# Kernel tuning notes

Hardware: AMD Instinct MI355X
Metric: run time of the kernel (lower is better)

## Reference

```python
import jax, jax.numpy as jnp
import numpy as np

N = 50000       # nodes
E = 800000      # directed edges (before self-loops)
IN = 128        # in_channels
H = 8           # heads
C = 32          # hidden_channels (per head)
OUT = 4         # out_channels
NS_ATT = 0.2    # PyG GATConv attention leaky-relu slope
NS_ACT = 0.01   # model activation leaky-relu slope
EPS = 1e-5      # BatchNorm eps


def setup_inputs() -> dict:
    key = jax.random.key(0)
    ks = jax.random.split(key, 18)
    s = 0.05
    return {
        "x": jax.random.normal(ks[0], (N, IN), jnp.float32),
        "edge_index": jax.random.randint(ks[1], (2, E), 0, N, dtype=jnp.int32),
        # layer 1: GATConv(IN -> C, heads=H, concat)
        "W1": jax.random.normal(ks[2], (IN, H * C), jnp.float32) * s,
        "as1": jax.random.normal(ks[3], (H, C), jnp.float32) * s,
        "ad1": jax.random.normal(ks[4], (H, C), jnp.float32) * s,
        "b1": jnp.zeros((H * C,), jnp.float32),
        "g1": jnp.ones((H * C,), jnp.float32),
        "be1": jnp.zeros((H * C,), jnp.float32),
        # middle layer: GATConv(H*C -> C, heads=H, concat) + BN + residual
        "W2": jax.random.normal(ks[5], (H * C, H * C), jnp.float32) * s,
        "as2": jax.random.normal(ks[6], (H, C), jnp.float32) * s,
        "ad2": jax.random.normal(ks[7], (H, C), jnp.float32) * s,
        "b2": jnp.zeros((H * C,), jnp.float32),
        "g2": jnp.ones((H * C,), jnp.float32),
        "be2": jnp.zeros((H * C,), jnp.float32),
        # final layer: GATConv(H*C -> OUT, heads=1, concat=False)
        "W3": jax.random.normal(ks[8], (H * C, OUT), jnp.float32) * s,
        "as3": jax.random.normal(ks[9], (1, OUT), jnp.float32) * s,
        "ad3": jax.random.normal(ks[10], (1, OUT), jnp.float32) * s,
        "b3": jnp.zeros((OUT,), jnp.float32),
    }


def _lrelu(x, slope):
    return jnp.where(x >= 0, x, slope * x)


def _gat_conv(x, src, dst, W, a_src, a_dst, bias, heads, ch, concat):
    # PyG GATConv: h = x @ W per head; edge logit = LReLU(a_src.h_j + a_dst.h_i)
    n = x.shape[0]
    h = (x @ W).reshape(n, heads, ch)                      # [N,H,C]
    al_s = jnp.sum(h * a_src, axis=-1)                     # [N,H]
    al_d = jnp.sum(h * a_dst, axis=-1)                     # [N,H]
    logits = _lrelu(al_s[src] + al_d[dst], NS_ATT)         # [E,H]
    # segment softmax over edges grouped by destination node
    m = jax.ops.segment_max(logits, dst, num_segments=n)   # [N,H]
    e = jnp.exp(logits - m[dst])
    denom = jax.ops.segment_sum(e, dst, num_segments=n)
    alpha = e / (denom[dst] + 1e-16)                       # [E,H]
    out = jax.ops.segment_sum(alpha[:, :, None] * h[src], dst, num_segments=n)  # [N,H,C]
    if concat:
        return out.reshape(n, heads * ch) + bias
    return out.mean(axis=1) + bias


def _bn(x, gamma, beta):
    mu = jnp.mean(x, axis=0)
    var = jnp.mean((x - mu) ** 2, axis=0)
    return (x - mu) * jax.lax.rsqrt(var + EPS) * gamma + beta


def reference(x, edge_index, W1, as1, ad1, b1, g1, be1,
              W2, as2, ad2, b2, g2, be2, W3, as3, ad3, b3):
    n = x.shape[0]
    loops = jnp.arange(n, dtype=edge_index.dtype)          # self-loops (PyG default)
    src = jnp.concatenate([edge_index[0], loops])
    dst = jnp.concatenate([edge_index[1], loops])
    h = _lrelu(_bn(_gat_conv(x, src, dst, W1, as1, ad1, b1, H, C, True), g1, be1), NS_ACT)
    residual = h
    h = _lrelu(_bn(_gat_conv(h, src, dst, W2, as2, ad2, b2, H, C, True), g2, be2), NS_ACT)
    h = h + residual
    return _gat_conv(h, src, dst, W3, as3, ad3, b3, 1, OUT, False)
```

## Files before the change

### kernel.cpp

```cpp
#include <hip/hip_runtime.h>

typedef __attribute__((ext_vector_type(8))) short bf16x8;
typedef __attribute__((ext_vector_type(4))) float f32x4;

__device__ __forceinline__ float lrelu(float x, float s) { return x >= 0.f ? x : s * x; }
__device__ __forceinline__ float b2f(unsigned short u) {
  union { unsigned int i; float f; } v; v.i = ((unsigned int)u) << 16; return v.f;
}
__device__ __forceinline__ float b2f_lo(unsigned int u) {
  union { unsigned int i; float f; } v; v.i = u << 16; return v.f;
}
__device__ __forceinline__ float b2f_hi(unsigned int u) {
  union { unsigned int i; float f; } v; v.i = u & 0xffff0000u; return v.f;
}
__device__ __forceinline__ unsigned short f2b(float f) {
  union { float f; unsigned int i; } v; v.f = f;
  unsigned int r = v.i + 0x7fffu + ((v.i >> 16) & 1u);
  return (unsigned short)(r >> 16);
}
__device__ __forceinline__ unsigned int fbits(float f) {
  union { float f; unsigned int i; } v; v.f = f; return v.i;
}
__device__ __forceinline__ float bitsf(unsigned int u) {
  union { unsigned int i; float f; } v; v.i = u; return v.f;
}

__global__ __launch_bounds__(256) void k_hist(const int* __restrict__ dst, int e,
                                              int* __restrict__ cnt) {
  int i = blockIdx.x * 256 + threadIdx.x;
  if (i < e) atomicAdd(&cnt[dst[i]], 1);
}

__global__ __launch_bounds__(256) void k_bsum(const int* __restrict__ cnt,
                                              int* __restrict__ bsum, int n) {
  const int base = blockIdx.x * 1024;
  const int t = threadIdx.x;
  int s = 0;
#pragma unroll
  for (int i = 0; i < 4; ++i) {
    int idx = base + t + i * 256;
    if (idx < n) s += cnt[idx] + 1;
  }
#pragma unroll
  for (int off = 1; off < 64; off <<= 1) s += __shfl_xor(s, off);
  __shared__ int ws[4];
  const int lane = t & 63, w = t >> 6;
  if (lane == 0) ws[w] = s;
  __syncthreads();
  if (t == 0) bsum[blockIdx.x] = ws[0] + ws[1] + ws[2] + ws[3];
}

__global__ __launch_bounds__(64) void k_scanb(const int* __restrict__ bsum,
                                              int* __restrict__ boff,
                                              int* __restrict__ ptrN, int B) {
  const int lane = threadIdx.x;
  int v = lane < B ? bsum[lane] : 0;
  int incl = v;
#pragma unroll
  for (int off = 1; off < 64; off <<= 1) {
    int u = __shfl_up(incl, off);
    if (lane >= off) incl += u;
  }
  if (lane < B) boff[lane] = incl - v;
  if (lane == 63) *ptrN = incl;
}

__global__ __launch_bounds__(256) void k_scanl(const int* __restrict__ cnt,
                                               const int* __restrict__ boff,
                                               int* __restrict__ ptr,
                                               int* __restrict__ fill, int n) {
  __shared__ int ws[4];
  const int t = threadIdx.x;
  const int base = blockIdx.x * 1024 + t * 4;
  int v0 = base + 0 < n ? cnt[base + 0] + 1 : 0;
  int v1 = base + 1 < n ? cnt[base + 1] + 1 : 0;
  int v2 = base + 2 < n ? cnt[base + 2] + 1 : 0;
  int v3 = base + 3 < n ? cnt[base + 3] + 1 : 0;
  const int tsum = v0 + v1 + v2 + v3;
  const int lane = t & 63, w = t >> 6;
  int incl = tsum;
#pragma unroll
  for (int off = 1; off < 64; off <<= 1) {
    int u = __shfl_up(incl, off);
    if (lane >= off) incl += u;
  }
  if (lane == 63) ws[w] = incl;
  __syncthreads();
  int excl = boff[blockIdx.x] + incl - tsum;
  for (int i = 0; i < w; ++i) excl += ws[i];
  if (base + 0 < n) { ptr[base + 0] = excl; fill[base + 0] = excl; }
  excl += v0;
  if (base + 1 < n) { ptr[base + 1] = excl; fill[base + 1] = excl; }
  excl += v1;
  if (base + 2 < n) { ptr[base + 2] = excl; fill[base + 2] = excl; }
  excl += v2;
  if (base + 3 < n) { ptr[base + 3] = excl; fill[base + 3] = excl; }
}

__global__ __launch_bounds__(256) void k_scatter(const int* __restrict__ srce,
                                                 const int* __restrict__ dste,
                                                 int e, int n,
                                                 int* __restrict__ fill,
                                                 int* __restrict__ srcs) {
  int i = blockIdx.x * 256 + threadIdx.x;
  if (i < e) {
    int pos = atomicAdd(&fill[dste[i]], 1);
    srcs[pos] = srce[i];
  } else if (i < e + n) {
    int v = i - e;
    int pos = atomicAdd(&fill[v], 1);
    srcs[pos] = v;
  }
}

__global__ __launch_bounds__(256) void k_prep(const float* __restrict__ x,
                                              unsigned short* __restrict__ xb,
                                              const float* __restrict__ W1,
                                              unsigned short* __restrict__ w1t,
                                              const float* __restrict__ W2,
                                              unsigned short* __restrict__ w2t, int n4) {
  int i = blockIdx.x * 256 + threadIdx.x;
  if (i < n4) {
    float4 v = ((const float4*)x)[i];
    ushort4 o;
    o.x = f2b(v.x); o.y = f2b(v.y); o.z = f2b(v.z); o.w = f2b(v.w);
    ((ushort4*)xb)[i] = o;
    return;
  }
  i -= n4;
  if (i < 256 * 128) {
    int nn = i / 128, k = i - nn * 128;
    w1t[i] = f2b(W1[(size_t)k * 256 + nn]);
    return;
  }
  i -= 256 * 128;
  if (i < 256 * 256) {
    int nn = i / 256, k = i - nn * 256;
    w2t[i] = f2b(W2[(size_t)k * 256 + nn]);
  }
}

__global__ __launch_bounds__(256) void k_mfma(const unsigned short* __restrict__ A,
                                              const unsigned short* __restrict__ BT,
                                              unsigned short* __restrict__ C,
                                              const float* __restrict__ as_,
                                              const float* __restrict__ ad_,
                                              float* __restrict__ als,
                                              float* __restrict__ ald,
                                              int M, int Nn, int K) {
  __shared__ unsigned int Asu[128 * 20];
  __shared__ unsigned int Bsu[128 * 20];
  const int tid = threadIdx.x;
  const int bm = blockIdx.x * 128, bn = blockIdx.y * 128;
  const int w = tid >> 6, lane = tid & 63;
  const int wm = w >> 1, wn = w & 1;
  const int l16 = lane & 15, lg = lane >> 4;
  f32x4 acc[4][4] = {};
  for (int k0 = 0; k0 < K; k0 += 32) {
#pragma unroll
    for (int rep = 0; rep < 2; ++rep) {
      int ci = tid + rep * 256;
      int row = ci >> 2, cg = ci & 3;
      int ar = bm + row;
      ar = ar < M ? ar : M - 1;
      uint4 av = *(const uint4*)(A + (size_t)ar * K + k0 + cg * 8);
      *(uint4*)&Asu[row * 20 + cg * 4] = av;
      uint4 bv = *(const uint4*)(BT + (size_t)(bn + row) * K + k0 + cg * 8);
      *(uint4*)&Bsu[row * 20 + cg * 4] = bv;
    }
    __syncthreads();
    bf16x8 aF[4], bF[4];
#pragma unroll
    for (int mi = 0; mi < 4; ++mi)
      aF[mi] = *(const bf16x8*)&Asu[(wm * 64 + mi * 16 + l16) * 20 + lg * 4];
#pragma unroll
    for (int ni = 0; ni < 4; ++ni)
      bF[ni] = *(const bf16x8*)&Bsu[(wn * 64 + ni * 16 + l16) * 20 + lg * 4];
#pragma unroll
    for (int mi = 0; mi < 4; ++mi)
#pragma unroll
      for (int ni = 0; ni < 4; ++ni)
        acc[mi][ni] =
            __builtin_amdgcn_mfma_f32_16x16x32_bf16(aF[mi], bF[ni], acc[mi][ni], 0, 0, 0);
    __syncthreads();
  }
  float asv[4], adv[4];
#pragma unroll
  for (int ni = 0; ni < 4; ++ni) {
    int gcol = bn + wn * 64 + ni * 16 + l16;
    asv[ni] = as_[gcol];
    adv[ni] = ad_[gcol];
  }
  const int hb = (bn >> 5) + wn * 2;
#pragma unroll
  for (int mi = 0; mi < 4; ++mi) {
#pragma unroll
    for (int r = 0; r < 4; ++r) {
      int grow = bm + wm * 64 + mi * 16 + lg * 4 + r;
      bool ok = grow < M;
      if (ok) {
#pragma unroll
        for (int ni = 0; ni < 4; ++ni) {
          int gcol = bn + wn * 64 + ni * 16 + l16;
          C[(size_t)grow * Nn + gcol] = f2b(acc[mi][ni][r]);
        }
      }
      float ps0 = acc[mi][0][r] * asv[0] + acc[mi][1][r] * asv[1];
      float ps1 = acc[mi][2][r] * asv[2] + acc[mi][3][r] * asv[3];
      float pd0 = acc[mi][0][r] * adv[0] + acc[mi][1][r] * adv[1];
      float pd1 = acc[mi][2][r] * adv[2] + acc[mi][3][r] * adv[3];
#pragma unroll
      for (int off = 1; off < 16; off <<= 1) {
        ps0 += __shfl_xor(ps0, off);
        ps1 += __shfl_xor(ps1, off);
        pd0 += __shfl_xor(pd0, off);
        pd1 += __shfl_xor(pd1, off);
      }
      if (ok && l16 == 0) {
        *(float2*)(als + (size_t)grow * 8 + hb) = make_float2(ps0, ps1);
        *(float2*)(ald + (size_t)grow * 8 + hb) = make_float2(pd0, pd1);
      }
    }
  }
}

__global__ __launch_bounds__(256) void k_agg(const unsigned short* __restrict__ h,
                                             const float* __restrict__ als,
                                             const float* __restrict__ ald,
                                             const int* __restrict__ ptr,
                                             const int* __restrict__ srcs,
                                             const float* __restrict__ bias,
                                             unsigned short* __restrict__ out, int n) {
  int wid = (blockIdx.x * 256 + threadIdx.x) >> 6;
  int lane = threadIdx.x & 63;
  if (wid >= n) return;
  const int beg = ptr[wid], end = ptr[wid + 1];
  const int L = lane & 15;
  const int e = lane >> 4;
  const int hh = L >> 1;
  const float adh = ald[(size_t)wid * 8 + hh];
  float s = 0.f;
  float a0 = 0, a1 = 0, a2 = 0, a3 = 0, a4 = 0, a5 = 0, a6 = 0, a7 = 0;
  float a8 = 0, a9 = 0, aA = 0, aB = 0, aC = 0, aD = 0, aE = 0, aF = 0;
  int j = beg + e;
  int s0 = j < end ? srcs[j] : 0;
  int s1 = (j + 4) < end ? srcs[j + 4] : 0;
  const uint4* hp0 = (const uint4*)(h + (size_t)s0 * 256 + L * 16);
  uint4 c0 = hp0[0];
  uint4 c1 = hp0[1];
  float alsc = als[(size_t)s0 * 8 + hh];
  for (; j < end; j += 4) {
    int s2 = (j + 8) < end ? srcs[j + 8] : 0;
    const uint4* hp1 = (const uint4*)(h + (size_t)s1 * 256 + L * 16);
    uint4 n0 = hp1[0];
    uint4 n1 = hp1[1];
    float alsn = als[(size_t)s1 * 8 + hh];
    float lg = lrelu(alsc + adh, 0.2f);
    float wt = __expf(lg);
    s += wt;
    a0 += wt * b2f_lo(c0.x); a1 += wt * b2f_hi(c0.x);
    a2 += wt * b2f_lo(c0.y); a3 += wt * b2f_hi(c0.y);
    a4 += wt * b2f_lo(c0.z); a5 += wt * b2f_hi(c0.z);
    a6 += wt * b2f_lo(c0.w); a7 += wt * b2f_hi(c0.w);
    a8 += wt * b2f_lo(c1.x); a9 += wt * b2f_hi(c1.x);
    aA += wt * b2f_lo(c1.y); aB += wt * b2f_hi(c1.y);
    aC += wt * b2f_lo(c1.z); aD += wt * b2f_hi(c1.z);
    aE += wt * b2f_lo(c1.w); aF += wt * b2f_hi(c1.w);
    c0 = n0; c1 = n1; alsc = alsn;
    s1 = s2;
  }
  a0 += __shfl_xor(a0, 16); a0 += __shfl_xor(a0, 32);
  a1 += __shfl_xor(a1, 16); a1 += __shfl_xor(a1, 32);
  a2 += __shfl_xor(a2, 16); a2 += __shfl_xor(a2, 32);
  a3 += __shfl_xor(a3, 16); a3 += __shfl_xor(a3, 32);
  a4 += __shfl_xor(a4, 16); a4 += __shfl_xor(a4, 32);
  a5 += __shfl_xor(a5, 16); a5 += __shfl_xor(a5, 32);
  a6 += __shfl_xor(a6, 16); a6 += __shfl_xor(a6, 32);
  a7 += __shfl_xor(a7, 16); a7 += __shfl_xor(a7, 32);
  a8 += __shfl_xor(a8, 16); a8 += __shfl_xor(a8, 32);
  a9 += __shfl_xor(a9, 16); a9 += __shfl_xor(a9, 32);
  aA += __shfl_xor(aA, 16); aA += __shfl_xor(aA, 32);
  aB += __shfl_xor(aB, 16); aB += __shfl_xor(aB, 32);
  aC += __shfl_xor(aC, 16); aC += __shfl_xor(aC, 32);
  aD += __shfl_xor(aD, 16); aD += __shfl_xor(aD, 32);
  aE += __shfl_xor(aE, 16); aE += __shfl_xor(aE, 32);
  aF += __shfl_xor(aF, 16); aF += __shfl_xor(aF, 32);
  s += __shfl_xor(s, 16); s += __shfl_xor(s, 32);
  const float inv = 1.f / (s + 1e-16f);
  if (e == 0) {
    const float4* bp = (const float4*)(bias + L * 16);
    float4 b0 = bp[0], b1 = bp[1], b2 = bp[2], b3 = bp[3];
    uint4 o0, o1;
    o0.x = (unsigned int)f2b(a0 * inv + b0.x) | ((unsigned int)f2b(a1 * inv + b0.y) << 16);
    o0.y = (unsigned int)f2b(a2 * inv + b0.z) | ((unsigned int)f2b(a3 * inv + b0.w) << 16);
    o0.z = (unsigned int)f2b(a4 * inv + b1.x) | ((unsigned int)f2b(a5 * inv + b1.y) << 16);
    o0.w = (unsigned int)f2b(a6 * inv + b1.z) | ((unsigned int)f2b(a7 * inv + b1.w) << 16);
    o1.x = (unsigned int)f2b(a8 * inv + b2.x) | ((unsigned int)f2b(a9 * inv + b2.y) << 16);
    o1.y = (unsigned int)f2b(aA * inv + b2.z) | ((unsigned int)f2b(aB * inv + b2.w) << 16);
    o1.z = (unsigned int)f2b(aC * inv + b3.x) | ((unsigned int)f2b(aD * inv + b3.y) << 16);
    o1.w = (unsigned int)f2b(aE * inv + b3.z) | ((unsigned int)f2b(aF * inv + b3.w) << 16);
    uint4* op = (uint4*)(out + (size_t)wid * 256 + L * 16);
    op[0] = o0;
    op[1] = o1;
  }
}

__global__ __launch_bounds__(256) void k_bnp1(const unsigned short* __restrict__ x,
                                              float* __restrict__ partial, int n) {
  const int t = threadIdx.x;
  const int q = t & 63;
  const int rsub = t >> 6;
  float s0 = 0, s1 = 0, s2 = 0, s3 = 0, q0 = 0, q1 = 0, q2 = 0, q3 = 0;
  int r = blockIdx.x * 4 + rsub;
  for (; r + 6144 < n; r += 8192) {
    ushort4 va = *(const ushort4*)(x + (size_t)r * 256 + q * 4);
    ushort4 vb = *(const ushort4*)(x + (size_t)(r + 2048) * 256 + q * 4);
    ushort4 vc = *(const ushort4*)(x + (size_t)(r + 4096) * 256 + q * 4);
    ushort4 vd = *(const ushort4*)(x + (size_t)(r + 6144) * 256 + q * 4);
    float f;
    f = b2f(va.x); s0 += f; q0 += f * f;
    f = b2f(va.y); s1 += f; q1 += f * f;
    f = b2f(va.z); s2 += f; q2 += f * f;
    f = b2f(va.w); s3 += f; q3 += f * f;
    f = b2f(vb.x); s0 += f; q0 += f * f;
    f = b2f(vb.y); s1 += f; q1 += f * f;
    f = b2f(vb.z); s2 += f; q2 += f * f;
    f = b2f(vb.w); s3 += f; q3 += f * f;
    f = b2f(vc.x); s0 += f; q0 += f * f;
    f = b2f(vc.y); s1 += f; q1 += f * f;
    f = b2f(vc.z); s2 += f; q2 += f * f;
    f = b2f(vc.w); s3 += f; q3 += f * f;
    f = b2f(vd.x); s0 += f; q0 += f * f;
    f = b2f(vd.y); s1 += f; q1 += f * f;
    f = b2f(vd.z); s2 += f; q2 += f * f;
    f = b2f(vd.w); s3 += f; q3 += f * f;
  }
  for (; r < n; r += 2048) {
    ushort4 v = *(const ushort4*)(x + (size_t)r * 256 + q * 4);
    float f;
    f = b2f(v.x); s0 += f; q0 += f * f;
    f = b2f(v.y); s1 += f; q1 += f * f;
    f = b2f(v.z); s2 += f; q2 += f * f;
    f = b2f(v.w); s3 += f; q3 += f * f;
  }
  __shared__ float ls[4][512];
  ls[rsub][q * 4 + 0] = s0; ls[rsub][q * 4 + 1] = s1;
  ls[rsub][q * 4 + 2] = s2; ls[rsub][q * 4 + 3] = s3;
  ls[rsub][256 + q * 4 + 0] = q0; ls[rsub][256 + q * 4 + 1] = q1;
  ls[rsub][256 + q * 4 + 2] = q2; ls[rsub][256 + q * 4 + 3] = q3;
  __syncthreads();
  float a = ls[0][t] + ls[1][t] + ls[2][t] + ls[3][t];
  float b = ls[0][256 + t] + ls[1][256 + t] + ls[2][256 + t] + ls[3][256 + t];
  partial[blockIdx.x * 512 + t] = a;
  partial[blockIdx.x * 512 + 256 + t] = b;
}

__global__ __launch_bounds__(256) void k_bnp2(const float* __restrict__ partial,
                                              const float* __restrict__ ga,
                                              const float* __restrict__ be,
                                              float* __restrict__ ss, float invn) {
  const int c = blockIdx.x * 4 + (threadIdx.x >> 6);
  const int lane = threadIdx.x & 63;
  float s = 0.f, qq = 0.f;
#pragma unroll
  for (int k = 0; k < 8; ++k) {
    int b = lane + k * 64;
    s += partial[(size_t)b * 512 + c];
    qq += partial[(size_t)b * 512 + 256 + c];
  }
#pragma unroll
  for (int off = 1; off < 64; off <<= 1) {
    s += __shfl_xor(s, off);
    qq += __shfl_xor(qq, off);
  }
  if (lane == 0) {
    float mu = s * invn;
    float var = qq * invn - mu * mu;
    float sc = ga[c] * rsqrtf(var + 1e-5f);
    ss[c] = sc;
    ss[256 + c] = be[c] - mu * sc;
  }
}

__global__ __launch_bounds__(256) void k_bnact(const unsigned short* __restrict__ x,
                                               const float* __restrict__ ss,
                                               unsigned short* __restrict__ out, int n) {
  const int tot4 = n * 64;
  for (int t = blockIdx.x * 256 + threadIdx.x; t < tot4; t += gridDim.x * 256) {
    int i0 = t * 4;
    int c = i0 & 255;
    ushort4 xu = *(const ushort4*)(x + i0);
    float4 scv = *(const float4*)(ss + c);
    float4 shv = *(const float4*)(ss + 256 + c);
    float t0 = b2f(xu.x) * scv.x + shv.x;
    float t1 = b2f(xu.y) * scv.y + shv.y;
    float t2 = b2f(xu.z) * scv.z + shv.z;
    float t3 = b2f(xu.w) * scv.w + shv.w;
    float o0 = fmaxf(t0, 0.01f * t0);
    float o1 = fmaxf(t1, 0.01f * t1);
    float o2 = fmaxf(t2, 0.01f * t2);
    float o3 = fmaxf(t3, 0.01f * t3);
    ushort4 ob;
    ob.x = f2b(o0); ob.y = f2b(o1); ob.z = f2b(o2); ob.w = f2b(o3);
    *(ushort4*)(out + i0) = ob;
  }
}

__global__ __launch_bounds__(256) void k_bnact3(const unsigned short* __restrict__ x,
                                                const float* __restrict__ ss,
                                                const unsigned short* __restrict__ res,
                                                const float* __restrict__ W3,
                                                const float* __restrict__ as3,
                                                const float* __restrict__ ad3,
                                                uint4* __restrict__ h3p, int n) {
  int wid = (blockIdx.x * 256 + threadIdx.x) >> 6;
  int lane = threadIdx.x & 63;
  if (wid >= n) return;
  const int c = lane * 4;
  ushort4 xu = *(const ushort4*)(x + (size_t)wid * 256 + c);
  ushort4 rv = *(const ushort4*)(res + (size_t)wid * 256 + c);
  float4 scv = *(const float4*)(ss + c);
  float4 shv = *(const float4*)(ss + 256 + c);
  float t0 = b2f(xu.x) * scv.x + shv.x;
  float t1 = b2f(xu.y) * scv.y + shv.y;
  float t2 = b2f(xu.z) * scv.z + shv.z;
  float t3 = b2f(xu.w) * scv.w + shv.w;
  float o0 = fmaxf(t0, 0.01f * t0) + b2f(rv.x);
  float o1 = fmaxf(t1, 0.01f * t1) + b2f(rv.y);
  float o2 = fmaxf(t2, 0.01f * t2) + b2f(rv.z);
  float o3 = fmaxf(t3, 0.01f * t3) + b2f(rv.w);
  const float4* Wp = (const float4*)W3 + lane * 4;
  float4 w0 = Wp[0], w1 = Wp[1], w2 = Wp[2], w3 = Wp[3];
  float a0 = o0 * w0.x + o1 * w1.x + o2 * w2.x + o3 * w3.x;
  float a1 = o0 * w0.y + o1 * w1.y + o2 * w2.y + o3 * w3.y;
  float a2 = o0 * w0.z + o1 * w1.z + o2 * w2.z + o3 * w3.z;
  float a3 = o0 * w0.w + o1 * w1.w + o2 * w2.w + o3 * w3.w;
#pragma unroll
  for (int off = 1; off < 64; off <<= 1) {
    a0 += __shfl_xor(a0, off);
    a1 += __shfl_xor(a1, off);
    a2 += __shfl_xor(a2, off);
    a3 += __shfl_xor(a3, off);
  }
  if (lane == 0) {
    float als3v = a0 * as3[0] + a1 * as3[1] + a2 * as3[2] + a3 * as3[3];
    float ald3v = a0 * ad3[0] + a1 * ad3[1] + a2 * ad3[2] + a3 * ad3[3];
    uint4 pv;
    pv.x = (unsigned int)f2b(a0) | ((unsigned int)f2b(a1) << 16);
    pv.y = (unsigned int)f2b(a2) | ((unsigned int)f2b(a3) << 16);
    pv.z = fbits(als3v);
    pv.w = fbits(ald3v);
    h3p[wid] = pv;
  }
}

__global__ __launch_bounds__(256) void k_agg3(const uint4* __restrict__ h3p,
                                              const int* __restrict__ ptr,
                                              const int* __restrict__ srcs,
                                              const float* __restrict__ b3,
                                              float* __restrict__ out, int n) {
  int wid = (blockIdx.x * 256 + threadIdx.x) >> 6;
  int lane = threadIdx.x & 63;
  if (wid >= n) return;
  const int beg = ptr[wid], end = ptr[wid + 1];
  const float aldh = bitsf(h3p[wid].w);
  float s = 0.f, a0 = 0.f, a1 = 0.f, a2 = 0.f, a3 = 0.f;
  for (int j = beg + lane; j < end; j += 64) {
    uint4 v = h3p[srcs[j]];
    float wgt = __expf(lrelu(bitsf(v.z) + aldh, 0.2f));
    s += wgt;
    a0 += wgt * b2f_lo(v.x);
    a1 += wgt * b2f_hi(v.x);
    a2 += wgt * b2f_lo(v.y);
    a3 += wgt * b2f_hi(v.y);
  }
#pragma unroll
  for (int off = 1; off < 64; off <<= 1) {
    s += __shfl_xor(s, off);
    a0 += __shfl_xor(a0, off);
    a1 += __shfl_xor(a1, off);
    a2 += __shfl_xor(a2, off);
    a3 += __shfl_xor(a3, off);
  }
  if (lane == 0) {
    float inv = 1.f / (s + 1e-16f);
    out[(size_t)wid * 4 + 0] = a0 * inv + b3[0];
    out[(size_t)wid * 4 + 1] = a1 * inv + b3[1];
    out[(size_t)wid * 4 + 2] = a2 * inv + b3[2];
    out[(size_t)wid * 4 + 3] = a3 * inv + b3[3];
  }
}

extern "C" void kernel_launch(void* const* d_in, const int* in_sizes, int n_in,
                              void* d_out, int out_size, void* d_ws, size_t ws_size,
                              hipStream_t stream) {
  const float* x   = (const float*)d_in[0];
  const int*   ei  = (const int*)d_in[1];
  const float* W1  = (const float*)d_in[2];
  const float* as1 = (const float*)d_in[3];
  const float* ad1 = (const float*)d_in[4];
  const float* b1  = (const float*)d_in[5];
  const float* ga1 = (const float*)d_in[6];
  const float* be1 = (const float*)d_in[7];
  const float* W2  = (const float*)d_in[8];
  const float* as2 = (const float*)d_in[9];
  const float* ad2 = (const float*)d_in[10];
  const float* b2  = (const float*)d_in[11];
  const float* ga2 = (const float*)d_in[12];
  const float* be2 = (const float*)d_in[13];
  const float* W3  = (const float*)d_in[14];
  const float* as3 = (const float*)d_in[15];
  const float* ad3 = (const float*)d_in[16];
  const float* b3  = (const float*)d_in[17];

  const int N = in_sizes[0] / 128;
  const int E = in_sizes[1] / 2;
  const int ET = E + N;
  float* out = (float*)d_out;

  char* w = (char*)d_ws;
  auto alloc = [&](size_t bytes) -> void* {
    void* p = (void*)w;
    w += (bytes + 255) & ~(size_t)255;
    return p;
  };
  int* ptr              = (int*)alloc((size_t)(N + 1) * 4);
  int* fill             = (int*)alloc((size_t)N * 4);
  int* cnt              = (int*)alloc((size_t)N * 4);
  int* bsum             = (int*)alloc(64 * 4);
  int* boff             = (int*)alloc(64 * 4);
  int* srcs             = (int*)alloc((size_t)ET * 4);
  unsigned short* hbuf  = (unsigned short*)alloc((size_t)N * 256 * 2);
  unsigned short* aggb  = (unsigned short*)alloc((size_t)N * 256 * 2);
  unsigned short* a1b   = (unsigned short*)alloc((size_t)N * 256 * 2);
  unsigned short* xb    = (unsigned short*)alloc((size_t)N * 128 * 2);
  unsigned short* w1t   = (unsigned short*)alloc(256 * 128 * 2);
  unsigned short* w2t   = (unsigned short*)alloc(256 * 256 * 2);
  float* als            = (float*)alloc((size_t)N * 8 * 4);
  float* ald            = (float*)alloc((size_t)N * 8 * 4);
  uint4* h3p            = (uint4*)alloc((size_t)N * 16);
  float* partial        = (float*)alloc(512 * 512 * 4);
  float* ss             = (float*)alloc(1024 * 4);

  const int* esrc = ei;
  const int* edst = ei + E;
  const float invn = 1.f / (float)N;

  hipMemsetAsync(cnt, 0, (size_t)N * 4, stream);

  const int B = (N + 1023) / 1024;
  k_hist<<<(E + 255) / 256, 256, 0, stream>>>(edst, E, cnt);
  k_bsum<<<B, 256, 0, stream>>>(cnt, bsum, N);
  k_scanb<<<1, 64, 0, stream>>>(bsum, boff, ptr + N, B);
  k_scanl<<<B, 256, 0, stream>>>(cnt, boff, ptr, fill, N);
  k_scatter<<<(ET + 255) / 256, 256, 0, stream>>>(esrc, edst, E, N, fill, srcs);

  const int n4 = N * 32;
  const int prep_tot = n4 + 256 * 128 + 256 * 256;
  k_prep<<<(prep_tot + 255) / 256, 256, 0, stream>>>(x, xb, W1, w1t, W2, w2t, n4);

  const dim3 gemm_grid((N + 127) / 128, 2);
  const int wblocks = (N + 3) / 4;

  k_mfma<<<gemm_grid, 256, 0, stream>>>(xb, w1t, hbuf, as1, ad1, als, ald, N, 256, 128);
  k_agg<<<wblocks, 256, 0, stream>>>(hbuf, als, ald, ptr, srcs, b1, aggb, N);
  k_bnp1<<<512, 256, 0, stream>>>(aggb, partial, N);
  k_bnp2<<<64, 256, 0, stream>>>(partial, ga1, be1, ss, invn);
  k_bnact<<<2048, 256, 0, stream>>>(aggb, ss, a1b, N);

  k_mfma<<<gemm_grid, 256, 0, stream>>>(a1b, w2t, hbuf, as2, ad2, als, ald, N, 256, 256);
  k_agg<<<wblocks, 256, 0, stream>>>(hbuf, als, ald, ptr, srcs, b2, aggb, N);
  k_bnp1<<<512, 256, 0, stream>>>(aggb, partial, N);
  k_bnp2<<<64, 256, 0, stream>>>(partial, ga2, be2, ss + 512, invn);
  k_bnact3<<<wblocks, 256, 0, stream>>>(aggb, ss + 512, a1b, W3, as3, ad3, h3p, N);

  k_agg3<<<wblocks, 256, 0, stream>>>(h3p, ptr, srcs, b3, out, N);
}
```

Before: 376.5 us.

## Fuse CSR build and BatchNorm stages into persistent kernels with grid barriers

Replaces the histogram, scan, scatter and bf16 prep kernels with one persistent 512-block kernel that uses software grid-wide barriers between phases. The two BatchNorm partial, finalize and apply kernel triples are also each fused into one persistent kernel with grid barriers. The aim is to remove many small kernel launches and their gaps. The cost is atomic spin barriers, whose correctness depends on all 512 blocks being co-resident, and the CSR phases now run on fewer threads than before.

```diff
diff --git a/kernel.cpp b/kernel.cpp
--- a/kernel.cpp
+++ b/kernel.cpp
@@ -25,118 +25,134 @@
   union { unsigned int i; float f; } v; v.i = u; return v.f;
 }
 
-__global__ __launch_bounds__(256) void k_hist(const int* __restrict__ dst, int e,
-                                              int* __restrict__ cnt) {
-  int i = blockIdx.x * 256 + threadIdx.x;
-  if (i < e) atomicAdd(&cnt[dst[i]], 1);
-}
-
-__global__ __launch_bounds__(256) void k_bsum(const int* __restrict__ cnt,
-                                              int* __restrict__ bsum, int n) {
-  const int base = blockIdx.x * 1024;
-  const int t = threadIdx.x;
-  int s = 0;
-#pragma unroll
-  for (int i = 0; i < 4; ++i) {
-    int idx = base + t + i * 256;
-    if (idx < n) s += cnt[idx] + 1;
-  }
-#pragma unroll
-  for (int off = 1; off < 64; off <<= 1) s += __shfl_xor(s, off);
+__device__ __forceinline__ void gbar(int* bar, int nb) {
+  __syncthreads();
+  if (threadIdx.x == 0) {
+    __threadfence();
+    int s0 = __hip_atomic_load(&bar[1], __ATOMIC_RELAXED, __HIP_MEMORY_SCOPE_AGENT);
+    int old = __hip_atomic_fetch_add(&bar[0], 1, __ATOMIC_ACQ_REL, __HIP_MEMORY_SCOPE_AGENT);
+    if (old == nb - 1) {
+      __hip_atomic_store(&bar[0], 0, __ATOMIC_RELAXED, __HIP_MEMORY_SCOPE_AGENT);
+      __hip_atomic_fetch_add(&bar[1], 1, __ATOMIC_RELEASE, __HIP_MEMORY_SCOPE_AGENT);
+    } else {
+      while (__hip_atomic_load(&bar[1], __ATOMIC_ACQUIRE, __HIP_MEMORY_SCOPE_AGENT) == s0) {}
+    }
+    __threadfence();
+  }
+  __syncthreads();
+}
+
+__global__ __launch_bounds__(256, 2) void k_csr(int* __restrict__ bar,
+                                                int* __restrict__ cnt,
+                                                const int* __restrict__ esrc,
+                                                const int* __restrict__ edst,
+                                                int E, int N,
+                                                const float* __restrict__ x,
+                                                unsigned short* __restrict__ xb,
+                                                const float* __restrict__ W1,
+                                                unsigned short* __restrict__ w1t,
+                                                const float* __restrict__ W2,
+                                                unsigned short* __restrict__ w2t,
+                                                int* __restrict__ bsum,
+                                                int* __restrict__ ptr,
+                                                int* __restrict__ fill,
+                                                int* __restrict__ srcs) {
+  const int NB = gridDim.x;
+  const int g0 = blockIdx.x * 256 + threadIdx.x;
+  const int gs = NB * 256;
+  const int n4 = N * 32;
   __shared__ int ws[4];
-  const int lane = t & 63, w = t >> 6;
-  if (lane == 0) ws[w] = s;
-  __syncthreads();
-  if (t == 0) bsum[blockIdx.x] = ws[0] + ws[1] + ws[2] + ws[3];
-}
-
-__global__ __launch_bounds__(64) void k_scanb(const int* __restrict__ bsum,
-                                              int* __restrict__ boff,
-                                              int* __restrict__ ptrN, int B) {
-  const int lane = threadIdx.x;
-  int v = lane < B ? bsum[lane] : 0;
-  int incl = v;
-#pragma unroll
-  for (int off = 1; off < 64; off <<= 1) {
-    int u = __shfl_up(incl, off);
-    if (lane >= off) incl += u;
-  }
-  if (lane < B) boff[lane] = incl - v;
-  if (lane == 63) *ptrN = incl;
-}
-
-__global__ __launch_bounds__(256) void k_scanl(const int* __restrict__ cnt,
-                                               const int* __restrict__ boff,
-                                               int* __restrict__ ptr,
-                                               int* __restrict__ fill, int n) {
-  __shared__ int ws[4];
-  const int t = threadIdx.x;
-  const int base = blockIdx.x * 1024 + t * 4;
-  int v0 = base + 0 < n ? cnt[base + 0] + 1 : 0;
-  int v1 = base + 1 < n ? cnt[base + 1] + 1 : 0;
-  int v2 = base + 2 < n ? cnt[base + 2] + 1 : 0;
-  int v3 = base + 3 < n ? cnt[base + 3] + 1 : 0;
-  const int tsum = v0 + v1 + v2 + v3;
-  const int lane = t & 63, w = t >> 6;
-  int incl = tsum;
-#pragma unroll
-  for (int off = 1; off < 64; off <<= 1) {
-    int u = __shfl_up(incl, off);
-    if (lane >= off) incl += u;
-  }
-  if (lane == 63) ws[w] = incl;
-  __syncthreads();
-  int excl = boff[blockIdx.x] + incl - tsum;
-  for (int i = 0; i < w; ++i) excl += ws[i];
-  if (base + 0 < n) { ptr[base + 0] = excl; fill[base + 0] = excl; }
-  excl += v0;
-  if (base + 1 < n) { ptr[base + 1] = excl; fill[base + 1] = excl; }
-  excl += v1;
-  if (base + 2 < n) { ptr[base + 2] = excl; fill[base + 2] = excl; }
-  excl += v2;
-  if (base + 3 < n) { ptr[base + 3] = excl; fill[base + 3] = excl; }
-}
-
-__global__ __launch_bounds__(256) void k_scatter(const int* __restrict__ srce,
-                                                 const int* __restrict__ dste,
-                                                 int e, int n,
-                                                 int* __restrict__ fill,
-                                                 int* __restrict__ srcs) {
-  int i = blockIdx.x * 256 + threadIdx.x;
-  if (i < e) {
-    int pos = atomicAdd(&fill[dste[i]], 1);
-    srcs[pos] = srce[i];
-  } else if (i < e + n) {
-    int v = i - e;
-    int pos = atomicAdd(&fill[v], 1);
-    srcs[pos] = v;
-  }
-}
-
-__global__ __launch_bounds__(256) void k_prep(const float* __restrict__ x,
-                                              unsigned short* __restrict__ xb,
-                                              const float* __restrict__ W1,
-                                              unsigned short* __restrict__ w1t,
-                                              const float* __restrict__ W2,
-                                              unsigned short* __restrict__ w2t, int n4) {
-  int i = blockIdx.x * 256 + threadIdx.x;
-  if (i < n4) {
+  __shared__ int bo_s;
+
+  for (int i = g0; i < N; i += gs) cnt[i] = 0;
+  for (int i = g0; i < n4; i += gs) {
     float4 v = ((const float4*)x)[i];
     ushort4 o;
     o.x = f2b(v.x); o.y = f2b(v.y); o.z = f2b(v.z); o.w = f2b(v.w);
     ((ushort4*)xb)[i] = o;
-    return;
-  }
-  i -= n4;
-  if (i < 256 * 128) {
-    int nn = i / 128, k = i - nn * 128;
+  }
+  for (int i = g0; i < 256 * 128; i += gs) {
+    int nn = i >> 7, k = i & 127;
     w1t[i] = f2b(W1[(size_t)k * 256 + nn]);
-    return;
-  }
-  i -= 256 * 128;
-  if (i < 256 * 256) {
-    int nn = i / 256, k = i - nn * 256;
+  }
+  for (int i = g0; i < 256 * 256; i += gs) {
+    int nn = i >> 8, k = i & 255;
     w2t[i] = f2b(W2[(size_t)k * 256 + nn]);
+  }
+  gbar(bar, NB);
+
+  for (int i = g0; i < E; i += gs) atomicAdd(&cnt[edst[i]], 1);
+  gbar(bar, NB);
+
+  const int B = (N + 1023) >> 10;
+  const int t = threadIdx.x;
+  if (blockIdx.x < B) {
+    const int base = blockIdx.x * 1024;
+    int s = 0;
+#pragma unroll
+    for (int i2 = 0; i2 < 4; ++i2) {
+      int idx = base + t + i2 * 256;
+      if (idx < N) s += cnt[idx] + 1;
+    }
+#pragma unroll
+    for (int off = 1; off < 64; off <<= 1) s += __shfl_xor(s, off);
+    const int lane = t & 63, w = t >> 6;
+    if (lane == 0) ws[w] = s;
+    __syncthreads();
+    if (t == 0) bsum[blockIdx.x] = ws[0] + ws[1] + ws[2] + ws[3];
+  }
+  gbar(bar, NB);
+
+  if (blockIdx.x < B) {
+    if (t < 64) {
+      int v = t < B ? bsum[t] : 0;
+      int incl = v;
+#pragma unroll
+      for (int off = 1; off < 64; off <<= 1) {
+        int u = __shfl_up(incl, off);
+        if (t >= off) incl += u;
+      }
+      if (t == blockIdx.x) bo_s = incl - v;
+      if (blockIdx.x == 0 && t == 63) ptr[N] = incl;
+    }
+    const int base = blockIdx.x * 1024 + t * 4;
+    int v0 = base + 0 < N ? cnt[base + 0] + 1 : 0;
+    int v1 = base + 1 < N ? cnt[base + 1] + 1 : 0;
+    int v2 = base + 2 < N ? cnt[base + 2] + 1 : 0;
+    int v3 = base + 3 < N ? cnt[base + 3] + 1 : 0;
+    const int tsum = v0 + v1 + v2 + v3;
+    const int lane = t & 63, w = t >> 6;
+    int incl = tsum;
+#pragma unroll
+    for (int off = 1; off < 64; off <<= 1) {
+      int u = __shfl_up(incl, off);
+      if (lane >= off) incl += u;
+    }
+    if (lane == 63) ws[w] = incl;
+    __syncthreads();
+    int excl = bo_s + incl - tsum;
+    for (int i = 0; i < w; ++i) excl += ws[i];
+    if (base + 0 < N) { ptr[base + 0] = excl; fill[base + 0] = excl; }
+    excl += v0;
+    if (base + 1 < N) { ptr[base + 1] = excl; fill[base + 1] = excl; }
+    excl += v1;
+    if (base + 2 < N) { ptr[base + 2] = excl; fill[base + 2] = excl; }
+    excl += v2;
+    if (base + 3 < N) { ptr[base + 3] = excl; fill[base + 3] = excl; }
+  }
+  gbar(bar, NB);
+
+  for (int i = g0; i < E + N; i += gs) {
+    if (i < E) {
+      int d = edst[i];
+      int sv = esrc[i];
+      int pos = atomicAdd(&fill[d], 1);
+      __builtin_nontemporal_store(sv, &srcs[pos]);
+    } else {
+      int v = i - E;
+      int pos = atomicAdd(&fill[v], 1);
+      __builtin_nontemporal_store(v, &srcs[pos]);
+    }
   }
 }
 
@@ -305,152 +321,235 @@
   }
 }
 
-__global__ __launch_bounds__(256) void k_bnp1(const unsigned short* __restrict__ x,
-                                              float* __restrict__ partial, int n) {
+__global__ __launch_bounds__(256, 2) void k_bn1(int* __restrict__ bar,
+                                                const unsigned short* __restrict__ xa,
+                                                float* __restrict__ partial,
+                                                const float* __restrict__ ga,
+                                                const float* __restrict__ be,
+                                                float* __restrict__ ss, float invn,
+                                                unsigned short* __restrict__ outb, int n) {
+  const int NB = gridDim.x;
   const int t = threadIdx.x;
-  const int q = t & 63;
-  const int rsub = t >> 6;
-  float s0 = 0, s1 = 0, s2 = 0, s3 = 0, q0 = 0, q1 = 0, q2 = 0, q3 = 0;
-  int r = blockIdx.x * 4 + rsub;
-  for (; r + 6144 < n; r += 8192) {
-    ushort4 va = *(const ushort4*)(x + (size_t)r * 256 + q * 4);
-    ushort4 vb = *(const ushort4*)(x + (size_t)(r + 2048) * 256 + q * 4);
-    ushort4 vc = *(const ushort4*)(x + (size_t)(r + 4096) * 256 + q * 4);
-    ushort4 vd = *(const ushort4*)(x + (size_t)(r + 6144) * 256 + q * 4);
-    float f;
-    f = b2f(va.x); s0 += f; q0 += f * f;
-    f = b2f(va.y); s1 += f; q1 += f * f;
-    f = b2f(va.z); s2 += f; q2 += f * f;
-    f = b2f(va.w); s3 += f; q3 += f * f;
-    f = b2f(vb.x); s0 += f; q0 += f * f;
-    f = b2f(vb.y); s1 += f; q1 += f * f;
-    f = b2f(vb.z); s2 += f; q2 += f * f;
-    f = b2f(vb.w); s3 += f; q3 += f * f;
-    f = b2f(vc.x); s0 += f; q0 += f * f;
-    f = b2f(vc.y); s1 += f; q1 += f * f;
-    f = b2f(vc.z); s2 += f; q2 += f * f;
-    f = b2f(vc.w); s3 += f; q3 += f * f;
-    f = b2f(vd.x); s0 += f; q0 += f * f;
-    f = b2f(vd.y); s1 += f; q1 += f * f;
-    f = b2f(vd.z); s2 += f; q2 += f * f;
-    f = b2f(vd.w); s3 += f; q3 += f * f;
-  }
-  for (; r < n; r += 2048) {
-    ushort4 v = *(const ushort4*)(x + (size_t)r * 256 + q * 4);
-    float f;
-    f = b2f(v.x); s0 += f; q0 += f * f;
-    f = b2f(v.y); s1 += f; q1 += f * f;
-    f = b2f(v.z); s2 += f; q2 += f * f;
-    f = b2f(v.w); s3 += f; q3 += f * f;
-  }
-  __shared__ float ls[4][512];
-  ls[rsub][q * 4 + 0] = s0; ls[rsub][q * 4 + 1] = s1;
-  ls[rsub][q * 4 + 2] = s2; ls[rsub][q * 4 + 3] = s3;
-  ls[rsub][256 + q * 4 + 0] = q0; ls[rsub][256 + q * 4 + 1] = q1;
-  ls[rsub][256 + q * 4 + 2] = q2; ls[rsub][256 + q * 4 + 3] = q3;
-  __syncthreads();
-  float a = ls[0][t] + ls[1][t] + ls[2][t] + ls[3][t];
-  float b = ls[0][256 + t] + ls[1][256 + t] + ls[2][256 + t] + ls[3][256 + t];
-  partial[blockIdx.x * 512 + t] = a;
-  partial[blockIdx.x * 512 + 256 + t] = b;
-}
-
-__global__ __launch_bounds__(256) void k_bnp2(const float* __restrict__ partial,
-                                              const float* __restrict__ ga,
-                                              const float* __restrict__ be,
-                                              float* __restrict__ ss, float invn) {
-  const int c = blockIdx.x * 4 + (threadIdx.x >> 6);
-  const int lane = threadIdx.x & 63;
-  float s = 0.f, qq = 0.f;
-#pragma unroll
-  for (int k = 0; k < 8; ++k) {
-    int b = lane + k * 64;
-    s += partial[(size_t)b * 512 + c];
-    qq += partial[(size_t)b * 512 + 256 + c];
-  }
-#pragma unroll
-  for (int off = 1; off < 64; off <<= 1) {
-    s += __shfl_xor(s, off);
-    qq += __shfl_xor(qq, off);
-  }
-  if (lane == 0) {
-    float mu = s * invn;
-    float var = qq * invn - mu * mu;
-    float sc = ga[c] * rsqrtf(var + 1e-5f);
-    ss[c] = sc;
-    ss[256 + c] = be[c] - mu * sc;
-  }
-}
-
-__global__ __launch_bounds__(256) void k_bnact(const unsigned short* __restrict__ x,
-                                               const float* __restrict__ ss,
-                                               unsigned short* __restrict__ out, int n) {
-  const int tot4 = n * 64;
-  for (int t = blockIdx.x * 256 + threadIdx.x; t < tot4; t += gridDim.x * 256) {
-    int i0 = t * 4;
-    int c = i0 & 255;
-    ushort4 xu = *(const ushort4*)(x + i0);
-    float4 scv = *(const float4*)(ss + c);
-    float4 shv = *(const float4*)(ss + 256 + c);
-    float t0 = b2f(xu.x) * scv.x + shv.x;
-    float t1 = b2f(xu.y) * scv.y + shv.y;
-    float t2 = b2f(xu.z) * scv.z + shv.z;
-    float t3 = b2f(xu.w) * scv.w + shv.w;
-    float o0 = fmaxf(t0, 0.01f * t0);
-    float o1 = fmaxf(t1, 0.01f * t1);
-    float o2 = fmaxf(t2, 0.01f * t2);
-    float o3 = fmaxf(t3, 0.01f * t3);
-    ushort4 ob;
-    ob.x = f2b(o0); ob.y = f2b(o1); ob.z = f2b(o2); ob.w = f2b(o3);
-    *(ushort4*)(out + i0) = ob;
-  }
-}
-
-__global__ __launch_bounds__(256) void k_bnact3(const unsigned short* __restrict__ x,
-                                                const float* __restrict__ ss,
+  {
+    const int q = t & 63;
+    const int rsub = t >> 6;
+    float s0 = 0, s1 = 0, s2 = 0, s3 = 0, q0 = 0, q1 = 0, q2 = 0, q3 = 0;
+    int r = blockIdx.x * 4 + rsub;
+    for (; r + 6144 < n; r += 8192) {
+      ushort4 va = *(const ushort4*)(xa + (size_t)r * 256 + q * 4);
+      ushort4 vb = *(const ushort4*)(xa + (size_t)(r + 2048) * 256 + q * 4);
+      ushort4 vc = *(const ushort4*)(xa + (size_t)(r + 4096) * 256 + q * 4);
+      ushort4 vd = *(const ushort4*)(xa + (size_t)(r + 6144) * 256 + q * 4);
+      float f;
+      f = b2f(va.x); s0 += f; q0 += f * f;
+      f = b2f(va.y); s1 += f; q1 += f * f;
+      f = b2f(va.z); s2 += f; q2 += f * f;
+      f = b2f(va.w); s3 += f; q3 += f * f;
+      f = b2f(vb.x); s0 += f; q0 += f * f;
+      f = b2f(vb.y); s1 += f; q1 += f * f;
+      f = b2f(vb.z); s2 += f; q2 += f * f;
+      f = b2f(vb.w); s3 += f; q3 += f * f;
+      f = b2f(vc.x); s0 += f; q0 += f * f;
+      f = b2f(vc.y); s1 += f; q1 += f * f;
+      f = b2f(vc.z); s2 += f; q2 += f * f;
+      f = b2f(vc.w); s3 += f; q3 += f * f;
+      f = b2f(vd.x); s0 += f; q0 += f * f;
+      f = b2f(vd.y); s1 += f; q1 += f * f;
+      f = b2f(vd.z); s2 += f; q2 += f * f;
+      f = b2f(vd.w); s3 += f; q3 += f * f;
+    }
+    for (; r < n; r += 2048) {
+      ushort4 v = *(const ushort4*)(xa + (size_t)r * 256 + q * 4);
+      float f;
+      f = b2f(v.x); s0 += f; q0 += f * f;
+      f = b2f(v.y); s1 += f; q1 += f * f;
+      f = b2f(v.z); s2 += f; q2 += f * f;
+      f = b2f(v.w); s3 += f; q3 += f * f;
+    }
+    __shared__ float ls[4][512];
+    ls[rsub][q * 4 + 0] = s0; ls[rsub][q * 4 + 1] = s1;
+    ls[rsub][q * 4 + 2] = s2; ls[rsub][q * 4 + 3] = s3;
+    ls[rsub][256 + q * 4 + 0] = q0; ls[rsub][256 + q * 4 + 1] = q1;
+    ls[rsub][256 + q * 4 + 2] = q2; ls[rsub][256 + q * 4 + 3] = q3;
+    __syncthreads();
+    float a = ls[0][t] + ls[1][t] + ls[2][t] + ls[3][t];
+    float b = ls[0][256 + t] + ls[1][256 + t] + ls[2][256 + t] + ls[3][256 + t];
+    partial[blockIdx.x * 512 + t] = a;
+    partial[blockIdx.x * 512 + 256 + t] = b;
+  }
+  gbar(bar, NB);
+  if (blockIdx.x < 64) {
+    const int c = blockIdx.x * 4 + (t >> 6);
+    const int lane = t & 63;
+    float s = 0.f, qq = 0.f;
+#pragma unroll
+    for (int k = 0; k < 8; ++k) {
+      int b = lane + k * 64;
+      s += partial[(size_t)b * 512 + c];
+      qq += partial[(size_t)b * 512 + 256 + c];
+    }
+#pragma unroll
+    for (int off = 1; off < 64; off <<= 1) {
+      s += __shfl_xor(s, off);
+      qq += __shfl_xor(qq, off);
+    }
+    if (lane == 0) {
+      float mu = s * invn;
+      float var = qq * invn - mu * mu;
+      float sc = ga[c] * rsqrtf(var + 1e-5f);
+      ss[c] = sc;
+      ss[256 + c] = be[c] - mu * sc;
+    }
+  }
+  gbar(bar, NB);
+  {
+    const int tot4 = n * 64;
+    for (int i = blockIdx.x * 256 + t; i < tot4; i += NB * 256) {
+      int i0 = i * 4;
+      int c = i0 & 255;
+      ushort4 xu = *(const ushort4*)(xa + i0);
+      float4 scv = *(const float4*)(ss + c);
+      float4 shv = *(const float4*)(ss + 256 + c);
+      float t0 = b2f(xu.x) * scv.x + shv.x;
+      float t1 = b2f(xu.y) * scv.y + shv.y;
+      float t2 = b2f(xu.z) * scv.z + shv.z;
+      float t3 = b2f(xu.w) * scv.w + shv.w;
+      float o0 = fmaxf(t0, 0.01f * t0);
+      float o1 = fmaxf(t1, 0.01f * t1);
+      float o2 = fmaxf(t2, 0.01f * t2);
+      float o3 = fmaxf(t3, 0.01f * t3);
+      ushort4 ob;
+      ob.x = f2b(o0); ob.y = f2b(o1); ob.z = f2b(o2); ob.w = f2b(o3);
+      *(ushort4*)(outb + i0) = ob;
+    }
+  }
+}
+
+__global__ __launch_bounds__(256, 2) void k_bn2(int* __restrict__ bar,
+                                                const unsigned short* __restrict__ xa,
+                                                float* __restrict__ partial,
+                                                const float* __restrict__ ga,
+                                                const float* __restrict__ be,
+                                                float* __restrict__ ss, float invn,
                                                 const unsigned short* __restrict__ res,
                                                 const float* __restrict__ W3,
                                                 const float* __restrict__ as3,
                                                 const float* __restrict__ ad3,
                                                 uint4* __restrict__ h3p, int n) {
-  int wid = (blockIdx.x * 256 + threadIdx.x) >> 6;
-  int lane = threadIdx.x & 63;
-  if (wid >= n) return;
-  const int c = lane * 4;
-  ushort4 xu = *(const ushort4*)(x + (size_t)wid * 256 + c);
-  ushort4 rv = *(const ushort4*)(res + (size_t)wid * 256 + c);
-  float4 scv = *(const float4*)(ss + c);
-  float4 shv = *(const float4*)(ss + 256 + c);
-  float t0 = b2f(xu.x) * scv.x + shv.x;
-  float t1 = b2f(xu.y) * scv.y + shv.y;
-  float t2 = b2f(xu.z) * scv.z + shv.z;
-  float t3 = b2f(xu.w) * scv.w + shv.w;
-  float o0 = fmaxf(t0, 0.01f * t0) + b2f(rv.x);
-  float o1 = fmaxf(t1, 0.01f * t1) + b2f(rv.y);
-  float o2 = fmaxf(t2, 0.01f * t2) + b2f(rv.z);
-  float o3 = fmaxf(t3, 0.01f * t3) + b2f(rv.w);
-  const float4* Wp = (const float4*)W3 + lane * 4;
-  float4 w0 = Wp[0], w1 = Wp[1], w2 = Wp[2], w3 = Wp[3];
-  float a0 = o0 * w0.x + o1 * w1.x + o2 * w2.x + o3 * w3.x;
-  float a1 = o0 * w0.y + o1 * w1.y + o2 * w2.y + o3 * w3.y;
-  float a2 = o0 * w0.z + o1 * w1.z + o2 * w2.z + o3 * w3.z;
-  float a3 = o0 * w0.w + o1 * w1.w + o2 * w2.w + o3 * w3.w;
-#pragma unroll
-  for (int off = 1; off < 64; off <<= 1) {
-    a0 += __shfl_xor(a0, off);
-    a1 += __shfl_xor(a1, off);
-    a2 += __shfl_xor(a2, off);
-    a3 += __shfl_xor(a3, off);
-  }
-  if (lane == 0) {
-    float als3v = a0 * as3[0] + a1 * as3[1] + a2 * as3[2] + a3 * as3[3];
-    float ald3v = a0 * ad3[0] + a1 * ad3[1] + a2 * ad3[2] + a3 * ad3[3];
-    uint4 pv;
-    pv.x = (unsigned int)f2b(a0) | ((unsigned int)f2b(a1) << 16);
-    pv.y = (unsigned int)f2b(a2) | ((unsigned int)f2b(a3) << 16);
-    pv.z = fbits(als3v);
-    pv.w = fbits(ald3v);
-    h3p[wid] = pv;
+  const int NB = gridDim.x;
+  const int t = threadIdx.x;
+  {
+    const int q = t & 63;
+    const int rsub = t >> 6;
+    float s0 = 0, s1 = 0, s2 = 0, s3 = 0, q0 = 0, q1 = 0, q2 = 0, q3 = 0;
+    int r = blockIdx.x * 4 + rsub;
+    for (; r + 6144 < n; r += 8192) {
+      ushort4 va = *(const ushort4*)(xa + (size_t)r * 256 + q * 4);
+      ushort4 vb = *(const ushort4*)(xa + (size_t)(r + 2048) * 256 + q * 4);
+      ushort4 vc = *(const ushort4*)(xa + (size_t)(r + 4096) * 256 + q * 4);
+      ushort4 vd = *(const ushort4*)(xa + (size_t)(r + 6144) * 256 + q * 4);
+      float f;
+      f = b2f(va.x); s0 += f; q0 += f * f;
+      f = b2f(va.y); s1 += f; q1 += f * f;
+      f = b2f(va.z); s2 += f; q2 += f * f;
+      f = b2f(va.w); s3 += f; q3 += f * f;
+      f = b2f(vb.x); s0 += f; q0 += f * f;
+      f = b2f(vb.y); s1 += f; q1 += f * f;
+      f = b2f(vb.z); s2 += f; q2 += f * f;
+      f = b2f(vb.w); s3 += f; q3 += f * f;
+      f = b2f(vc.x); s0 += f; q0 += f * f;
+      f = b2f(vc.y); s1 += f; q1 += f * f;
+      f = b2f(vc.z); s2 += f; q2 += f * f;
+      f = b2f(vc.w); s3 += f; q3 += f * f;
+      f = b2f(vd.x); s0 += f; q0 += f * f;
+      f = b2f(vd.y); s1 += f; q1 += f * f;
+      f = b2f(vd.z); s2 += f; q2 += f * f;
+      f = b2f(vd.w); s3 += f; q3 += f * f;
+    }
+    for (; r < n; r += 2048) {
+      ushort4 v = *(const ushort4*)(xa + (size_t)r * 256 + q * 4);
+      float f;
+      f = b2f(v.x); s0 += f; q0 += f * f;
+      f = b2f(v.y); s1 += f; q1 += f * f;
+      f = b2f(v.z); s2 += f; q2 += f * f;
+      f = b2f(v.w); s3 += f; q3 += f * f;
+    }
+    __shared__ float ls[4][512];
+    ls[rsub][q * 4 + 0] = s0; ls[rsub][q * 4 + 1] = s1;
+    ls[rsub][q * 4 + 2] = s2; ls[rsub][q * 4 + 3] = s3;
+    ls[rsub][256 + q * 4 + 0] = q0; ls[rsub][256 + q * 4 + 1] = q1;
+    ls[rsub][256 + q * 4 + 2] = q2; ls[rsub][256 + q * 4 + 3] = q3;
+    __syncthreads();
+    float a = ls[0][t] + ls[1][t] + ls[2][t] + ls[3][t];
+    float b = ls[0][256 + t] + ls[1][256 + t] + ls[2][256 + t] + ls[3][256 + t];
+    partial[blockIdx.x * 512 + t] = a;
+    partial[blockIdx.x * 512 + 256 + t] = b;
+  }
+  gbar(bar, NB);
+  if (blockIdx.x < 64) {
+    const int c = blockIdx.x * 4 + (t >> 6);
+    const int lane = t & 63;
+    float s = 0.f, qq = 0.f;
+#pragma unroll
+    for (int k = 0; k < 8; ++k) {
+      int b = lane + k * 64;
+      s += partial[(size_t)b * 512 + c];
+      qq += partial[(size_t)b * 512 + 256 + c];
+    }
+#pragma unroll
+    for (int off = 1; off < 64; off <<= 1) {
+      s += __shfl_xor(s, off);
+      qq += __shfl_xor(qq, off);
+    }
+    if (lane == 0) {
+      float mu = s * invn;
+      float var = qq * invn - mu * mu;
+      float sc = ga[c] * rsqrtf(var + 1e-5f);
+      ss[c] = sc;
+      ss[256 + c] = be[c] - mu * sc;
+    }
+  }
+  gbar(bar, NB);
+  {
+    const int lane = t & 63;
+    const int c = lane * 4;
+    const float4* Wp = (const float4*)W3 + lane * 4;
+    float4 w0 = Wp[0], w1 = Wp[1], w2 = Wp[2], w3 = Wp[3];
+    float4 scv = *(const float4*)(ss + c);
+    float4 shv = *(const float4*)(ss + 256 + c);
+    for (int wid = blockIdx.x * 4 + (t >> 6); wid < n; wid += NB * 4) {
+      ushort4 xu = *(const ushort4*)(xa + (size_t)wid * 256 + c);
+      ushort4 rv = *(const ushort4*)(res + (size_t)wid * 256 + c);
+      float t0 = b2f(xu.x) * scv.x + shv.x;
+      float t1 = b2f(xu.y) * scv.y + shv.y;
+      float t2 = b2f(xu.z) * scv.z + shv.z;
+      float t3 = b2f(xu.w) * scv.w + shv.w;
+      float o0 = fmaxf(t0, 0.01f * t0) + b2f(rv.x);
+      float o1 = fmaxf(t1, 0.01f * t1) + b2f(rv.y);
+      float o2 = fmaxf(t2, 0.01f * t2) + b2f(rv.z);
+      float o3 = fmaxf(t3, 0.01f * t3) + b2f(rv.w);
+      float a0 = o0 * w0.x + o1 * w1.x + o2 * w2.x + o3 * w3.x;
+      float a1 = o0 * w0.y + o1 * w1.y + o2 * w2.y + o3 * w3.y;
+      float a2 = o0 * w0.z + o1 * w1.z + o2 * w2.z + o3 * w3.z;
+      float a3 = o0 * w0.w + o1 * w1.w + o2 * w2.w + o3 * w3.w;
+#pragma unroll
+      for (int off = 1; off < 64; off <<= 1) {
+        a0 += __shfl_xor(a0, off);
+        a1 += __shfl_xor(a1, off);
+        a2 += __shfl_xor(a2, off);
+        a3 += __shfl_xor(a3, off);
+      }
+      if (lane == 0) {
+        float als3v = a0 * as3[0] + a1 * as3[1] + a2 * as3[2] + a3 * as3[3];
+        float ald3v = a0 * ad3[0] + a1 * ad3[1] + a2 * ad3[2] + a3 * ad3[3];
+        uint4 pv;
+        pv.x = (unsigned int)f2b(a0) | ((unsigned int)f2b(a1) << 16);
+        pv.y = (unsigned int)f2b(a2) | ((unsigned int)f2b(a3) << 16);
+        pv.z = fbits(als3v);
+        pv.w = fbits(ald3v);
+        h3p[wid] = pv;
+      }
+    }
   }
 }
 
@@ -524,11 +623,11 @@
     w += (bytes + 255) & ~(size_t)255;
     return p;
   };
+  int* bar              = (int*)alloc(6 * 4);
   int* ptr              = (int*)alloc((size_t)(N + 1) * 4);
   int* fill             = (int*)alloc((size_t)N * 4);
   int* cnt              = (int*)alloc((size_t)N * 4);
   int* bsum             = (int*)alloc(64 * 4);
-  int* boff             = (int*)alloc(64 * 4);
   int* srcs             = (int*)alloc((size_t)ET * 4);
   unsigned short* hbuf  = (unsigned short*)alloc((size_t)N * 256 * 2);
   unsigned short* aggb  = (unsigned short*)alloc((size_t)N * 256 * 2);
@@ -546,33 +645,22 @@
   const int* edst = ei + E;
   const float invn = 1.f / (float)N;
 
-  hipMemsetAsync(cnt, 0, (size_t)N * 4, stream);
-
-  const int B = (N + 1023) / 1024;
-  k_hist<<<(E + 255) / 256, 256, 0, stream>>>(edst, E, cnt);
-  k_bsum<<<B, 256, 0, stream>>>(cnt, bsum, N);
-  k_scanb<<<1, 64, 0, stream>>>(bsum, boff, ptr + N, B);
-  k_scanl<<<B, 256, 0, stream>>>(cnt, boff, ptr, fill, N);
-  k_scatter<<<(ET + 255) / 256, 256, 0, stream>>>(esrc, edst, E, N, fill, srcs);
-
-  const int n4 = N * 32;
-  const int prep_tot = n4 + 256 * 128 + 256 * 256;
-  k_prep<<<(prep_tot + 255) / 256, 256, 0, stream>>>(x, xb, W1, w1t, W2, w2t, n4);
+  hipMemsetAsync(bar, 0, 6 * 4, stream);
+
+  k_csr<<<512, 256, 0, stream>>>(bar, cnt, esrc, edst, E, N, x, xb, W1, w1t, W2, w2t,
+                                 bsum, ptr, fill, srcs);
 
   const dim3 gemm_grid((N + 127) / 128, 2);
   const int wblocks = (N + 3) / 4;
 
   k_mfma<<<gemm_grid, 256, 0, stream>>>(xb, w1t, hbuf, as1, ad1, als, ald, N, 256, 128);
   k_agg<<<wblocks, 256, 0, stream>>>(hbuf, als, ald, ptr, srcs, b1, aggb, N);
-  k_bnp1<<<512, 256, 0, stream>>>(aggb, partial, N);
-  k_bnp2<<<64, 256, 0, stream>>>(partial, ga1, be1, ss, invn);
-  k_bnact<<<2048, 256, 0, stream>>>(aggb, ss, a1b, N);
+  k_bn1<<<512, 256, 0, stream>>>(bar + 2, aggb, partial, ga1, be1, ss, invn, a1b, N);
 
   k_mfma<<<gemm_grid, 256, 0, stream>>>(a1b, w2t, hbuf, as2, ad2, als, ald, N, 256, 256);
   k_agg<<<wblocks, 256, 0, stream>>>(hbuf, als, ald, ptr, srcs, b2, aggb, N);
-  k_bnp1<<<512, 256, 0, stream>>>(aggb, partial, N);
-  k_bnp2<<<64, 256, 0, stream>>>(partial, ga2, be2, ss + 512, invn);
-  k_bnact3<<<wblocks, 256, 0, stream>>>(aggb, ss + 512, a1b, W3, as3, ad3, h3p, N);
+  k_bn2<<<512, 256, 0, stream>>>(bar + 4, aggb, partial, ga2, be2, ss + 512, invn,
+                                 a1b, W3, as3, ad3, h3p, N);
 
   k_agg3<<<wblocks, 256, 0, stream>>>(h3p, ptr, srcs, b3, out, N);
 }
```

Measured after the change: 1.050 ms. 179% more time.
